# Kernel optimization log

Hardware: AMD Instinct MI355X
Metric: run time of the kernel (lower is better)

The kernel has to match this reference:

```python
import jax, jax.numpy as jnp
import numpy as np

B, S, D, H = 2, 2048, 1024, 16
DK = D // H


def setup_inputs() -> dict:
    key = jax.random.key(0)
    ks = jax.random.split(key, 12)
    scale = 0.02  # keep exp(QK^T) finite in fp32
    return {
        "query": jax.random.normal(ks[0], (B, S, D), jnp.float32),
        "key_": jax.random.normal(ks[1], (B, S, D), jnp.float32),
        "value": jax.random.normal(ks[2], (B, S, D), jnp.float32),
        "mask": jax.random.randint(ks[3], (B, S, S), 0, 2, jnp.int32),
        "Wq": scale * jax.random.normal(ks[4], (D, D), jnp.float32),
        "bq": jnp.zeros((D,), jnp.float32),
        "Wk": scale * jax.random.normal(ks[5], (D, D), jnp.float32),
        "bk": jnp.zeros((D,), jnp.float32),
        "Wv": scale * jax.random.normal(ks[6], (D, D), jnp.float32),
        "bv": jnp.zeros((D,), jnp.float32),
        "Wo": scale * jax.random.normal(ks[7], (D, D), jnp.float32),
        "bo": jnp.zeros((D,), jnp.float32),
    }


def reference(query, key_, value, mask, Wq, bq, Wk, bk, Wv, bv, Wo, bo):
    b, s, d = query.shape
    # torch Linear: x @ W.T + b, then split heads -> [b, h, s, d_k]
    def proj(x, W, bias):
        return (x @ W.T + bias).reshape(b, s, H, DK).transpose(0, 2, 1, 3)

    q = proj(query, Wq, bq)
    k = proj(key_, Wk, bk)
    v = proj(value, Wv, bv)

    # non-standard: exp(QK^T) / sqrt(d_k), then mask, then softmax
    scores = jnp.exp(jnp.einsum("bhqd,bhkd->bhqk", q, k)) / jnp.sqrt(
        jnp.asarray(DK, q.dtype)
    )
    scores = jnp.where(mask[:, None, :, :] == 0, jnp.asarray(-1e9, q.dtype), scores)
    p_attn = jax.nn.softmax(scores, axis=-1)

    out = jnp.einsum("bhqk,bhkd->bhqd", p_attn, v)  # [b, h, s, d_k]
    out = out.transpose(0, 2, 1, 3).reshape(b, s, d)  # merge heads
    return out @ Wo.T + bo
```

## Files before the change

### kernel.cpp

```cpp
#include <hip/hip_runtime.h>
#include <math.h>

#define B_ 2
#define S_ 2048
#define D_ 1024
#define H_ 16
#define DK_ 64
#define M_ (B_*S_)

typedef __attribute__((ext_vector_type(8))) _Float16 f16x8;
typedef __attribute__((ext_vector_type(4))) _Float16 f16x4;
typedef __attribute__((ext_vector_type(2))) __fp16 fp16x2;
typedef __attribute__((ext_vector_type(4))) float f32x4;

#define MFMA16(a,b,c) __builtin_amdgcn_mfma_f32_16x16x32_f16((a),(b),(c),0,0,0)

__device__ __forceinline__ void gload16(const void* g, void* l) {
    __builtin_amdgcn_global_load_lds(
        (const __attribute__((address_space(1))) unsigned int*)g,
        (__attribute__((address_space(3))) unsigned int*)l, 16, 0, 0);
}

__global__ __launch_bounds__(256)
void wsplit(const float* __restrict__ Wq, const float* __restrict__ Wk,
            const float* __restrict__ Wv, const float* __restrict__ Wo,
            _Float16* __restrict__ hq, _Float16* __restrict__ lq,
            _Float16* __restrict__ hk, _Float16* __restrict__ lk,
            _Float16* __restrict__ hv, _Float16* __restrict__ ho)
{
    int t = blockIdx.x * 256 + threadIdx.x;
    int mi = t >> 17;
    int e  = (t & 131071) * 8;
    const float* src = (mi == 0) ? Wq : (mi == 1) ? Wk : (mi == 2) ? Wv : Wo;
    float4 a = *(const float4*)&src[e];
    float4 b = *(const float4*)&src[e + 4];
    float v[8] = {a.x, a.y, a.z, a.w, b.x, b.y, b.z, b.w};
    f16x8 hi, lo;
    #pragma unroll
    for (int j = 0; j < 8; ++j) {
        float s = v[j] * 64.f;
        _Float16 h = (_Float16)s;
        hi[j] = h; lo[j] = (_Float16)(s - (float)h);
    }
    if (mi == 0)      { *(f16x8*)&hq[e] = hi; *(f16x8*)&lq[e] = lo; }
    else if (mi == 1) { *(f16x8*)&hk[e] = hi; *(f16x8*)&lk[e] = lo; }
    else if (mi == 2) { *(f16x8*)&hv[e] = hi; }
    else              { *(f16x8*)&ho[e] = hi; }
}

__global__ __launch_bounds__(256)
void maskpack(const int* __restrict__ mask, unsigned long long* __restrict__ mbits)
{
    int wid  = (blockIdx.x * 256 + threadIdx.x) >> 6;
    int lane = threadIdx.x & 63;
    int v = mask[(size_t)wid * 64 + lane];
    unsigned long long bal = __ballot(v != 0);
    if (lane == 0) mbits[wid] = bal;
}

template<int NPROD, int OUT_MODE>
__device__ __forceinline__
void gemm_body(char* smem, const float* __restrict__ Ap,
               const _Float16* __restrict__ Bhi, const _Float16* __restrict__ Blo,
               const float* __restrict__ bias, void* __restrict__ outp, int gid)
{
    _Float16* AhiS = (_Float16*)smem;
    _Float16* BhiS = (_Float16*)(smem + 8192);
    _Float16* AloS = (_Float16*)(smem + 16384);
    _Float16* BloS = (_Float16*)(smem + 24576);

    const int tid  = threadIdx.x;
    const int lane = tid & 63, w = tid >> 6;
    const int lx   = lane & 15, lg = lane >> 4;
    const int wm   = w >> 1, wn = w & 1;

    int nid = (gid & 7) * 32 + (gid >> 3);
    const int colBase = (nid & 7) * 128;
    const int rowBase = (nid >> 3) * 128;

    f32x4 acc[4][4];
    #pragma unroll
    for (int i = 0; i < 4; ++i)
        #pragma unroll
        for (int j = 0; j < 4; ++j) acc[i][j] = (f32x4){0.f, 0.f, 0.f, 0.f};

    const int sr = tid >> 1, sh = tid & 1;

    for (int k0 = 0; k0 < D_; k0 += 32) {
        __syncthreads();
        #pragma unroll
        for (int ii = 0; ii < 2; ++ii) {
            int i  = w * 2 + ii;
            int rr = i * 16 + (lane >> 2);
            int cc = (lane & 3) ^ ((lane >> 2) & 3);
            gload16(Bhi + (size_t)(colBase + rr) * D_ + k0 + cc * 8, &BhiS[i * 512]);
            if (NPROD == 3)
                gload16(Blo + (size_t)(colBase + rr) * D_ + k0 + cc * 8, &BloS[i * 512]);
        }
        {
            char* bp = (char*)AhiS + sr * 64;
            int c0 = sh * 2;
            const float* ap = Ap + (size_t)(rowBase + sr) * D_ + k0 + sh * 16;
            float4 x0 = *(const float4*)ap;
            float4 x1 = *(const float4*)(ap + 4);
            float4 x2 = *(const float4*)(ap + 8);
            float4 x3 = *(const float4*)(ap + 12);
            float xv[16] = {x0.x,x0.y,x0.z,x0.w, x1.x,x1.y,x1.z,x1.w,
                            x2.x,x2.y,x2.z,x2.w, x3.x,x3.y,x3.z,x3.w};
            f16x8 hi[2], lo[2];
            #pragma unroll
            for (int j = 0; j < 16; ++j) {
                _Float16 hv = (_Float16)xv[j];
                hi[j >> 3][j & 7] = hv;
                if (NPROD == 3) lo[j >> 3][j & 7] = (_Float16)(xv[j] - (float)hv);
            }
            *(f16x8*)(bp + 16 * ((c0 + 0) ^ (sr & 3))) = hi[0];
            *(f16x8*)(bp + 16 * ((c0 + 1) ^ (sr & 3))) = hi[1];
            if (NPROD == 3) {
                char* lp = (char*)AloS + sr * 64;
                *(f16x8*)(lp + 16 * ((c0 + 0) ^ (sr & 3))) = lo[0];
                *(f16x8*)(lp + 16 * ((c0 + 1) ^ (sr & 3))) = lo[1];
            }
        }
        __syncthreads();

        f16x8 bh[4], bl[4];
        #pragma unroll
        for (int fj = 0; fj < 4; ++fj) {
            int brow = wn * 64 + fj * 16 + lx;
            bh[fj] = *(const f16x8*)((char*)BhiS + brow * 64 + 16 * (lg ^ (brow & 3)));
            if (NPROD == 3)
                bl[fj] = *(const f16x8*)((char*)BloS + brow * 64 + 16 * (lg ^ (brow & 3)));
        }
        #pragma unroll
        for (int fi = 0; fi < 4; ++fi) {
            int arow = wm * 64 + fi * 16 + lx;
            f16x8 ah = *(const f16x8*)((char*)AhiS + arow * 64 + 16 * (lg ^ (arow & 3)));
            f16x8 al;
            if (NPROD == 3)
                al = *(const f16x8*)((char*)AloS + arow * 64 + 16 * (lg ^ (arow & 3)));
            #pragma unroll
            for (int fj = 0; fj < 4; ++fj) {
                acc[fi][fj] = MFMA16(ah, bh[fj], acc[fi][fj]);
                if (NPROD == 3) {
                    acc[fi][fj] = MFMA16(ah, bl[fj], acc[fi][fj]);
                    acc[fi][fj] = MFMA16(al, bh[fj], acc[fi][fj]);
                }
            }
        }
    }

    constexpr float INV = 1.f / 64.f;
    #pragma unroll
    for (int fi = 0; fi < 4; ++fi) {
        #pragma unroll
        for (int fj = 0; fj < 4; ++fj) {
            int n = colBase + wn * 64 + fj * 16 + lx;
            float bv = bias[n];
            if (OUT_MODE == 1) {
                _Float16* Ohi = (_Float16*)outp;
                _Float16* Olo = Ohi + (size_t)M_ * D_;
                int hh = n >> 6, d = n & 63;
                #pragma unroll
                for (int rr = 0; rr < 4; ++rr) {
                    int m = rowBase + wm * 64 + fi * 16 + lg * 4 + rr;
                    int bb = m >> 11, s = m & 2047;
                    float val = acc[fi][fj][rr] * INV + bv;
                    _Float16 hv = (_Float16)val;
                    size_t o = (((size_t)bb * H_ + hh) * S_ + s) * DK_ + d;
                    Ohi[o] = hv;
                    Olo[o] = (_Float16)(val - (float)hv);
                }
            } else {
                _Float16* Vt = (_Float16*)outp;
                int hh = n >> 6, d = n & 63;
                int m0 = rowBase + wm * 64 + fi * 16 + lg * 4;
                int bb = m0 >> 11, s = m0 & 2047;
                f16x4 pk;
                #pragma unroll
                for (int rr = 0; rr < 4; ++rr)
                    pk[rr] = (_Float16)(acc[fi][fj][rr] * INV + bv);
                *(f16x4*)&Vt[(((size_t)bb * H_ + hh) * DK_ + d) * S_ + s] = pk;
            }
        }
    }
}

__global__ __launch_bounds__(256)
void proj3(const float* __restrict__ query, const float* __restrict__ key_,
           const float* __restrict__ value,
           const _Float16* __restrict__ WhiQ, const _Float16* __restrict__ WloQ,
           const _Float16* __restrict__ WhiK, const _Float16* __restrict__ WloK,
           const _Float16* __restrict__ WhiV,
           const float* __restrict__ bq, const float* __restrict__ bk,
           const float* __restrict__ bv,
           _Float16* __restrict__ Qhi, _Float16* __restrict__ Khi,
           _Float16* __restrict__ VtW)
{
    extern __shared__ char smem[];
    int mode = blockIdx.x >> 8;
    int gid  = blockIdx.x & 255;
    if (mode == 0)
        gemm_body<3, 1>(smem, query, WhiQ, WloQ, bq, Qhi, gid);
    else if (mode == 1)
        gemm_body<3, 1>(smem, key_, WhiK, WloK, bk, Khi, gid);
    else
        gemm_body<1, 2>(smem, value, WhiV, nullptr, bv, VtW, gid);
}

__global__ __launch_bounds__(256)
void gemm64(const _Float16* __restrict__ Ap, const _Float16* __restrict__ Bhi,
            const float* __restrict__ bias, float* __restrict__ out)
{
    __shared__ __attribute__((aligned(16))) _Float16 AhiS[64 * 32];
    __shared__ __attribute__((aligned(16))) _Float16 BhiS[128 * 32];

    const int tid  = threadIdx.x;
    const int lane = tid & 63, w = tid >> 6;
    const int lx   = lane & 15, lg = lane >> 4;
    const int wm   = w >> 1, wn = w & 1;

    int gid = blockIdx.x;
    int nid = (gid & 7) * 64 + (gid >> 3);
    const int colBase = (nid & 7) * 128;
    const int rowBase = (nid >> 3) * 64;

    f32x4 acc[2][4];
    #pragma unroll
    for (int i = 0; i < 2; ++i)
        #pragma unroll
        for (int j = 0; j < 4; ++j) acc[i][j] = (f32x4){0.f, 0.f, 0.f, 0.f};

    const int sr = tid >> 2, sh = tid & 3;

    for (int k0 = 0; k0 < D_; k0 += 32) {
        __syncthreads();
        #pragma unroll
        for (int ii = 0; ii < 2; ++ii) {
            int i  = w * 2 + ii;
            int rr = i * 16 + (lane >> 2);
            int cc = (lane & 3) ^ ((lane >> 2) & 3);
            gload16(Bhi + (size_t)(colBase + rr) * D_ + k0 + cc * 8, &BhiS[i * 512]);
        }
        {
            const _Float16* ap = Ap + (size_t)(rowBase + sr) * D_ + k0 + sh * 8;
            f16x8 h0 = *(const f16x8*)ap;
            *(f16x8*)((char*)AhiS + sr * 64 + 16 * (sh ^ (sr & 3))) = h0;
        }
        __syncthreads();

        f16x8 bh[4];
        #pragma unroll
        for (int fj = 0; fj < 4; ++fj) {
            int brow = wn * 64 + fj * 16 + lx;
            bh[fj] = *(const f16x8*)((char*)BhiS + brow * 64 + 16 * (lg ^ (brow & 3)));
        }
        #pragma unroll
        for (int fi = 0; fi < 2; ++fi) {
            int arow = wm * 32 + fi * 16 + lx;
            f16x8 ah = *(const f16x8*)((char*)AhiS + arow * 64 + 16 * (lg ^ (arow & 3)));
            #pragma unroll
            for (int fj = 0; fj < 4; ++fj)
                acc[fi][fj] = MFMA16(ah, bh[fj], acc[fi][fj]);
        }
    }

    constexpr float INV = 1.f / 64.f;
    #pragma unroll
    for (int fi = 0; fi < 2; ++fi) {
        #pragma unroll
        for (int fj = 0; fj < 4; ++fj) {
            int n = colBase + wn * 64 + fj * 16 + lx;
            float bv = bias[n];
            #pragma unroll
            for (int rr = 0; rr < 4; ++rr) {
                int m = rowBase + wm * 32 + fi * 16 + lg * 4 + rr;
                out[(size_t)m * D_ + n] = acc[fi][fj][rr] * INV + bv;
            }
        }
    }
}

__global__ __launch_bounds__(512, 4)
void flash_mfma(const _Float16* __restrict__ Qhi, const _Float16* __restrict__ Qlo,
                const _Float16* __restrict__ Khi, const _Float16* __restrict__ Klo,
                const _Float16* __restrict__ Vt, const unsigned long long* __restrict__ Mb,
                _Float16* __restrict__ octx)
{
    __shared__ __attribute__((aligned(16))) _Float16 KhiS[64 * 64];
    __shared__ __attribute__((aligned(16))) _Float16 KloS[64 * 64];
    __shared__ __attribute__((aligned(16))) _Float16 VtS[64 * 64];
    __shared__ __attribute__((aligned(16))) _Float16 PwS[8][16 * 64];

    const int tid  = threadIdx.x;
    const int lane = tid & 63;
    const int w    = tid >> 6;
    const int lx   = lane & 15;
    const int lg   = lane >> 4;

    int bid = blockIdx.x;
    int swz = (bid & 7) * 64 + (bid >> 3);
    int qb = swz & 15;
    int h  = (swz >> 4) & 15;
    int b  = swz >> 8;

    const int q0 = qb * 128;
    const size_t bh = (size_t)b * H_ + h;
    const _Float16* KhiG = Khi + bh * S_ * DK_;
    const _Float16* KloG = Klo + bh * S_ * DK_;
    const _Float16* VtG  = Vt  + bh * DK_ * S_;

    const int qrow = q0 + w * 16 + lx;
    f16x8 qh[2], ql[2];
    {
        const _Float16* ph = Qhi + bh * S_ * DK_ + (size_t)qrow * DK_ + lg * 8;
        const _Float16* pl = Qlo + bh * S_ * DK_ + (size_t)qrow * DK_ + lg * 8;
        qh[0] = *(const f16x8*)ph;
        qh[1] = *(const f16x8*)(ph + 32);
        ql[0] = *(const f16x8*)pl;
        ql[1] = *(const f16x8*)(pl + 32);
    }

    f32x4 oacc[4];
    float m_run = -1e30f, l_run = 0.f;
    #pragma unroll
    for (int dt = 0; dt < 4; ++dt) oacc[dt] = (f32x4){0.f, 0.f, 0.f, 0.f};

    char* Pw = (char*)&PwS[w][0];
    const unsigned long long* mrow = Mb + ((size_t)b * S_ + qrow) * (S_ / 64);

    for (int s0 = 0; s0 < S_; s0 += 64) {
        __syncthreads();

        {
            int rr = w * 8 + (lane >> 3);
            int cc = (lane & 7) ^ (lane >> 3);
            gload16(KhiG + (size_t)(s0 + rr) * DK_ + cc * 8, &KhiS[w * 512]);
            gload16(KloG + (size_t)(s0 + rr) * DK_ + cc * 8, &KloS[w * 512]);
            gload16(VtG + (size_t)rr * S_ + s0 + cc * 8, &VtS[w * 512]);
        }
        unsigned long long mw = mrow[s0 >> 6];
        __syncthreads();

        float sv[4][4];
        #pragma unroll
        for (int ct = 0; ct < 4; ++ct) {
            int row  = ct * 16 + lx;
            int sw   = (row & 7) << 4;
            int base = row * 128 + lg * 16;
            f16x8 kh0 = *(const f16x8*)((const char*)KhiS + ((base +  0) ^ sw));
            f16x8 kh1 = *(const f16x8*)((const char*)KhiS + ((base + 64) ^ sw));
            f16x8 kl0 = *(const f16x8*)((const char*)KloS + ((base +  0) ^ sw));
            f16x8 kl1 = *(const f16x8*)((const char*)KloS + ((base + 64) ^ sw));
            f32x4 s = (f32x4){0.f, 0.f, 0.f, 0.f};
            s = MFMA16(kh0, qh[0], s);
            s = MFMA16(kh1, qh[1], s);
            s = MFMA16(kl0, qh[0], s);
            s = MFMA16(kl1, qh[1], s);
            s = MFMA16(kh0, ql[0], s);
            s = MFMA16(kh1, ql[1], s);
            #pragma unroll
            for (int r = 0; r < 4; ++r) sv[ct][r] = s[r];
        }

        unsigned long long ms = mw >> (lg * 4);
        float tv[16];
        #pragma unroll
        for (int ct = 0; ct < 4; ++ct)
            #pragma unroll
            for (int r = 0; r < 4; ++r) {
                float e = __expf(sv[ct][r] - 2.0794415416798357f);
                tv[ct * 4 + r] = ((ms >> (ct * 16 + r)) & 1ull) ? e : -1e30f;
            }
        float m01 = fmaxf(fmaxf(tv[0], tv[1]), fmaxf(tv[2], tv[3]));
        float m23 = fmaxf(fmaxf(tv[4], tv[5]), fmaxf(tv[6], tv[7]));
        float m45 = fmaxf(fmaxf(tv[8], tv[9]), fmaxf(tv[10], tv[11]));
        float m67 = fmaxf(fmaxf(tv[12], tv[13]), fmaxf(tv[14], tv[15]));
        float tmax = fmaxf(fmaxf(m01, m23), fmaxf(m45, m67));
        tmax = fmaxf(tmax, __shfl_xor(tmax, 16));
        tmax = fmaxf(tmax, __shfl_xor(tmax, 32));

        if (__any(tmax > m_run)) {
            float mn = fmaxf(m_run, tmax);
            float scl = __expf(m_run - mn);
            m_run = mn;
            l_run *= scl;
            #pragma unroll
            for (int dt = 0; dt < 4; ++dt)
                #pragma unroll
                for (int r = 0; r < 4; ++r) oacc[dt][r] *= scl;
        }
        float mr = m_run;
        float pp[16], sum = 0.f;
        #pragma unroll
        for (int i = 0; i < 16; ++i) {
            pp[i] = __expf(tv[i] - mr);
            sum += pp[i];
        }
        sum += __shfl_xor(sum, 16);
        sum += __shfl_xor(sum, 32);
        l_run += sum;

        {
            int psw = (lx & 7) << 4;
            #pragma unroll
            for (int ct = 0; ct < 4; ++ct) {
                fp16x2 a = __builtin_amdgcn_cvt_pkrtz(pp[ct * 4 + 0], pp[ct * 4 + 1]);
                fp16x2 c = __builtin_amdgcn_cvt_pkrtz(pp[ct * 4 + 2], pp[ct * 4 + 3]);
                unsigned int au, cu;
                __builtin_memcpy(&au, &a, 4);
                __builtin_memcpy(&cu, &c, 4);
                int off = lx * 128 + ct * 32 + lg * 8;
                *(unsigned int*)(Pw + ((off + 0) ^ psw)) = au;
                *(unsigned int*)(Pw + ((off + 4) ^ psw)) = cu;
            }
        }

        f16x8 pa0, pa1;
        {
            int psw = (lx & 7) << 4;
            int pb  = lx * 128 + lg * 16;
            pa0 = *(const f16x8*)(Pw + ((pb +  0) ^ psw));
            pa1 = *(const f16x8*)(Pw + ((pb + 64) ^ psw));
        }
        #pragma unroll
        for (int dt = 0; dt < 4; ++dt) {
            int vrow = dt * 16 + lx;
            int vs   = (vrow & 7) << 4;
            int vb   = vrow * 128 + lg * 16;
            f16x8 v0 = *(const f16x8*)((const char*)VtS + ((vb +  0) ^ vs));
            f16x8 v1 = *(const f16x8*)((const char*)VtS + ((vb + 64) ^ vs));
            oacc[dt] = MFMA16(v0, pa0, oacc[dt]);
            oacc[dt] = MFMA16(v1, pa1, oacc[dt]);
        }
    }

    {
        float inv = 1.0f / l_run;
        #pragma unroll
        for (int dt = 0; dt < 4; ++dt) {
            f16x4 o;
            #pragma unroll
            for (int r = 0; r < 4; ++r) o[r] = (_Float16)(oacc[dt][r] * inv);
            *(f16x4*)&octx[((size_t)b * S_ + qrow) * D_ + h * DK_ + dt * 16 + lg * 4] = o;
        }
    }
}

extern "C" void kernel_launch(void* const* d_in, const int* in_sizes, int n_in,
                              void* d_out, int out_size, void* d_ws, size_t ws_size,
                              hipStream_t stream)
{
    const float* query = (const float*)d_in[0];
    const float* key_  = (const float*)d_in[1];
    const float* value = (const float*)d_in[2];
    const int*   mask  = (const int*)d_in[3];
    const float* Wq = (const float*)d_in[4];
    const float* bq = (const float*)d_in[5];
    const float* Wk = (const float*)d_in[6];
    const float* bk = (const float*)d_in[7];
    const float* Wv = (const float*)d_in[8];
    const float* bv = (const float*)d_in[9];
    const float* Wo = (const float*)d_in[10];
    const float* bo = (const float*)d_in[11];

    char* p = (char*)d_ws;
    unsigned long long* mbits = (unsigned long long*)p;  p += (size_t)1 << 20;
    _Float16* WhiQ = (_Float16*)p;  p += (size_t)2 << 20;
    _Float16* WloQ = (_Float16*)p;  p += (size_t)2 << 20;
    _Float16* WhiK = (_Float16*)p;  p += (size_t)2 << 20;
    _Float16* WloK = (_Float16*)p;  p += (size_t)2 << 20;
    _Float16* WhiV = (_Float16*)p;  p += (size_t)2 << 20;
    _Float16* WhiO = (_Float16*)p;  p += (size_t)2 << 20;
    _Float16* Qhi  = (_Float16*)p;  p += (size_t)8 << 20;
    _Float16* Qlo  = (_Float16*)p;  p += (size_t)8 << 20;
    _Float16* Khi  = (_Float16*)p;  p += (size_t)8 << 20;
    _Float16* Klo  = (_Float16*)p;  p += (size_t)8 << 20;
    _Float16* VtW  = (_Float16*)p;  p += (size_t)8 << 20;
    _Float16* octx = (_Float16*)p;  p += (size_t)8 << 20;
    float* out = (float*)d_out;
    (void)Qlo; (void)Klo;

    maskpack<<<(B_ * S_ * (S_ / 64) * 64) / 256, 256, 0, stream>>>(mask, mbits);
    wsplit<<<2048, 256, 0, stream>>>(Wq, Wk, Wv, Wo,
                                     WhiQ, WloQ, WhiK, WloK, WhiV, WhiO);

    proj3<<<768, 256, 32768, stream>>>(query, key_, value,
                                       WhiQ, WloQ, WhiK, WloK, WhiV,
                                       bq, bk, bv, Qhi, Khi, VtW);

    flash_mfma<<<512, 512, 0, stream>>>(Qhi, Qlo, Khi, Klo, VtW, mbits, octx);

    gemm64<<<512, 256, 0, stream>>>(octx, WhiO, bo, out);
}
```

Before: 225.1 us.

## Pre-split activations to fp16 and double-buffer LDS staging in projection GEMMs

Activations (query/key/value) are now pre-converted to fp16 hi/lo pairs, with a 64x scale, in a merged split kernel. The projection GEMM can then stage both A and B through async global_load_lds instead of converting fp32 in registers on every k-step. Both the projection GEMM and the output GEMM switch to double-buffered LDS, prefetching the next k-tile while computing the current one, which also removes one barrier per iteration. The cost is an extra full pass over the activations to write the fp16 copies, plus twice the LDS per block, which may lower occupancy. Qlo/Klo are now placed right after Qhi/Khi to match the OUT_MODE layout.

```diff
diff --git a/kernel.cpp b/kernel.cpp
--- a/kernel.cpp
+++ b/kernel.cpp
@@ -22,16 +22,33 @@
 }
 
 __global__ __launch_bounds__(256)
-void wsplit(const float* __restrict__ Wq, const float* __restrict__ Wk,
-            const float* __restrict__ Wv, const float* __restrict__ Wo,
-            _Float16* __restrict__ hq, _Float16* __restrict__ lq,
-            _Float16* __restrict__ hk, _Float16* __restrict__ lk,
-            _Float16* __restrict__ hv, _Float16* __restrict__ ho)
+void splitall(const float* __restrict__ query, const float* __restrict__ key_,
+              const float* __restrict__ value,
+              const float* __restrict__ Wq, const float* __restrict__ Wk,
+              const float* __restrict__ Wv, const float* __restrict__ Wo,
+              _Float16* __restrict__ Xhq, _Float16* __restrict__ Xlq,
+              _Float16* __restrict__ Xhk, _Float16* __restrict__ Xlk,
+              _Float16* __restrict__ Xhv,
+              _Float16* __restrict__ hq, _Float16* __restrict__ lq,
+              _Float16* __restrict__ hk, _Float16* __restrict__ lk,
+              _Float16* __restrict__ hv, _Float16* __restrict__ ho)
 {
     int t = blockIdx.x * 256 + threadIdx.x;
-    int mi = t >> 17;
-    int e  = (t & 131071) * 8;
-    const float* src = (mi == 0) ? Wq : (mi == 1) ? Wk : (mi == 2) ? Wv : Wo;
+    int region = t >> 19;
+    int u = t & 524287;
+    const float* src; _Float16* dhi; _Float16* dlo; size_t e;
+    if (region < 3) {
+        e = (size_t)u * 8;
+        src = (region == 0) ? query : (region == 1) ? key_ : value;
+        dhi = (region == 0) ? Xhq : (region == 1) ? Xhk : Xhv;
+        dlo = (region == 0) ? Xlq : (region == 1) ? Xlk : nullptr;
+    } else {
+        int mi = u >> 17;
+        e = (size_t)(u & 131071) * 8;
+        src = (mi == 0) ? Wq : (mi == 1) ? Wk : (mi == 2) ? Wv : Wo;
+        dhi = (mi == 0) ? hq : (mi == 1) ? hk : (mi == 2) ? hv : ho;
+        dlo = (mi == 0) ? lq : (mi == 1) ? lk : nullptr;
+    }
     float4 a = *(const float4*)&src[e];
     float4 b = *(const float4*)&src[e + 4];
     float v[8] = {a.x, a.y, a.z, a.w, b.x, b.y, b.z, b.w};
@@ -42,10 +59,8 @@
         _Float16 h = (_Float16)s;
         hi[j] = h; lo[j] = (_Float16)(s - (float)h);
     }
-    if (mi == 0)      { *(f16x8*)&hq[e] = hi; *(f16x8*)&lq[e] = lo; }
-    else if (mi == 1) { *(f16x8*)&hk[e] = hi; *(f16x8*)&lk[e] = lo; }
-    else if (mi == 2) { *(f16x8*)&hv[e] = hi; }
-    else              { *(f16x8*)&ho[e] = hi; }
+    *(f16x8*)&dhi[e] = hi;
+    if (dlo) *(f16x8*)&dlo[e] = lo;
 }
 
 __global__ __launch_bounds__(256)
@@ -60,15 +75,12 @@
 
 template<int NPROD, int OUT_MODE>
 __device__ __forceinline__
-void gemm_body(char* smem, const float* __restrict__ Ap,
-               const _Float16* __restrict__ Bhi, const _Float16* __restrict__ Blo,
-               const float* __restrict__ bias, void* __restrict__ outp, int gid)
-{
-    _Float16* AhiS = (_Float16*)smem;
-    _Float16* BhiS = (_Float16*)(smem + 8192);
-    _Float16* AloS = (_Float16*)(smem + 16384);
-    _Float16* BloS = (_Float16*)(smem + 24576);
-
+void gemm_body2(char* smem, const _Float16* __restrict__ Ah,
+                const _Float16* __restrict__ Al,
+                const _Float16* __restrict__ Bh, const _Float16* __restrict__ Bl,
+                const float* __restrict__ bias, void* __restrict__ outp, int gid)
+{
+    constexpr int BUFSZ = (NPROD == 3) ? 32768 : 16384;
     const int tid  = threadIdx.x;
     const int lane = tid & 63, w = tid >> 6;
     const int lx   = lane & 15, lg = lane >> 4;
@@ -78,67 +90,56 @@
     const int colBase = (nid & 7) * 128;
     const int rowBase = (nid >> 3) * 128;
 
+    const int sRow = (lane >> 2);
+    const int sChk = (lane & 3) ^ ((lane >> 2) & 3);
+
+    auto STAGE = [&](int buf, int k0) {
+        char* base = smem + buf * BUFSZ;
+        #pragma unroll
+        for (int ii = 0; ii < 2; ++ii) {
+            int i = w * 2 + ii;
+            int r = i * 16 + sRow;
+            gload16(Ah + (size_t)(rowBase + r) * D_ + k0 + sChk * 8, base + i * 1024);
+            gload16(Bh + (size_t)(colBase + r) * D_ + k0 + sChk * 8, base + 8192 + i * 1024);
+            if (NPROD == 3) {
+                gload16(Al + (size_t)(rowBase + r) * D_ + k0 + sChk * 8, base + 16384 + i * 1024);
+                gload16(Bl + (size_t)(colBase + r) * D_ + k0 + sChk * 8, base + 24576 + i * 1024);
+            }
+        }
+    };
+
     f32x4 acc[4][4];
     #pragma unroll
     for (int i = 0; i < 4; ++i)
         #pragma unroll
         for (int j = 0; j < 4; ++j) acc[i][j] = (f32x4){0.f, 0.f, 0.f, 0.f};
 
-    const int sr = tid >> 1, sh = tid & 1;
-
+    STAGE(0, 0);
+    __syncthreads();
+    int cur = 0;
     for (int k0 = 0; k0 < D_; k0 += 32) {
-        __syncthreads();
-        #pragma unroll
-        for (int ii = 0; ii < 2; ++ii) {
-            int i  = w * 2 + ii;
-            int rr = i * 16 + (lane >> 2);
-            int cc = (lane & 3) ^ ((lane >> 2) & 3);
-            gload16(Bhi + (size_t)(colBase + rr) * D_ + k0 + cc * 8, &BhiS[i * 512]);
-            if (NPROD == 3)
-                gload16(Blo + (size_t)(colBase + rr) * D_ + k0 + cc * 8, &BloS[i * 512]);
-        }
-        {
-            char* bp = (char*)AhiS + sr * 64;
-            int c0 = sh * 2;
-            const float* ap = Ap + (size_t)(rowBase + sr) * D_ + k0 + sh * 16;
-            float4 x0 = *(const float4*)ap;
-            float4 x1 = *(const float4*)(ap + 4);
-            float4 x2 = *(const float4*)(ap + 8);
-            float4 x3 = *(const float4*)(ap + 12);
-            float xv[16] = {x0.x,x0.y,x0.z,x0.w, x1.x,x1.y,x1.z,x1.w,
-                            x2.x,x2.y,x2.z,x2.w, x3.x,x3.y,x3.z,x3.w};
-            f16x8 hi[2], lo[2];
-            #pragma unroll
-            for (int j = 0; j < 16; ++j) {
-                _Float16 hv = (_Float16)xv[j];
-                hi[j >> 3][j & 7] = hv;
-                if (NPROD == 3) lo[j >> 3][j & 7] = (_Float16)(xv[j] - (float)hv);
-            }
-            *(f16x8*)(bp + 16 * ((c0 + 0) ^ (sr & 3))) = hi[0];
-            *(f16x8*)(bp + 16 * ((c0 + 1) ^ (sr & 3))) = hi[1];
-            if (NPROD == 3) {
-                char* lp = (char*)AloS + sr * 64;
-                *(f16x8*)(lp + 16 * ((c0 + 0) ^ (sr & 3))) = lo[0];
-                *(f16x8*)(lp + 16 * ((c0 + 1) ^ (sr & 3))) = lo[1];
-            }
-        }
-        __syncthreads();
+        if (k0 + 32 < D_) STAGE(cur ^ 1, k0 + 32);
+        char* base = smem + cur * BUFSZ;
+        _Float16* AhS = (_Float16*)base;
+        _Float16* BhS = (_Float16*)(base + 8192);
+        _Float16* AlS = (_Float16*)(base + 16384);
+        _Float16* BlS = (_Float16*)(base + 24576);
 
         f16x8 bh[4], bl[4];
         #pragma unroll
         for (int fj = 0; fj < 4; ++fj) {
             int brow = wn * 64 + fj * 16 + lx;
-            bh[fj] = *(const f16x8*)((char*)BhiS + brow * 64 + 16 * (lg ^ (brow & 3)));
+            bh[fj] = *(const f16x8*)((char*)BhS + brow * 64 + 16 * (lg ^ (brow & 3)));
             if (NPROD == 3)
-                bl[fj] = *(const f16x8*)((char*)BloS + brow * 64 + 16 * (lg ^ (brow & 3)));
+                bl[fj] = *(const f16x8*)((char*)BlS + brow * 64 + 16 * (lg ^ (brow & 3)));
         }
         #pragma unroll
         for (int fi = 0; fi < 4; ++fi) {
             int arow = wm * 64 + fi * 16 + lx;
-            f16x8 ah = *(const f16x8*)((char*)AhiS + arow * 64 + 16 * (lg ^ (arow & 3)));
+            f16x8 ah = *(const f16x8*)((char*)AhS + arow * 64 + 16 * (lg ^ (arow & 3)));
             f16x8 al;
             if (NPROD == 3)
-                al = *(const f16x8*)((char*)AloS + arow * 64 + 16 * (lg ^ (arow & 3)));
+                al = *(const f16x8*)((char*)AlS + arow * 64 + 16 * (lg ^ (arow & 3)));
             #pragma unroll
             for (int fj = 0; fj < 4; ++fj) {
                 acc[fi][fj] = MFMA16(ah, bh[fj], acc[fi][fj]);
@@ -148,9 +149,11 @@
                 }
             }
         }
-    }
-
-    constexpr float INV = 1.f / 64.f;
+        __syncthreads();
+        cur ^= 1;
+    }
+
+    constexpr float INV = 1.f / 4096.f;
     #pragma unroll
     for (int fi = 0; fi < 4; ++fi) {
         #pragma unroll
@@ -187,8 +190,9 @@
 }
 
 __global__ __launch_bounds__(256)
-void proj3(const float* __restrict__ query, const float* __restrict__ key_,
-           const float* __restrict__ value,
+void proj3(const _Float16* __restrict__ Xhq, const _Float16* __restrict__ Xlq,
+           const _Float16* __restrict__ Xhk, const _Float16* __restrict__ Xlk,
+           const _Float16* __restrict__ Xhv,
            const _Float16* __restrict__ WhiQ, const _Float16* __restrict__ WloQ,
            const _Float16* __restrict__ WhiK, const _Float16* __restrict__ WloK,
            const _Float16* __restrict__ WhiV,
@@ -201,19 +205,18 @@
     int mode = blockIdx.x >> 8;
     int gid  = blockIdx.x & 255;
     if (mode == 0)
-        gemm_body<3, 1>(smem, query, WhiQ, WloQ, bq, Qhi, gid);
+        gemm_body2<3, 1>(smem, Xhq, Xlq, WhiQ, WloQ, bq, Qhi, gid);
     else if (mode == 1)
-        gemm_body<3, 1>(smem, key_, WhiK, WloK, bk, Khi, gid);
+        gemm_body2<3, 1>(smem, Xhk, Xlk, WhiK, WloK, bk, Khi, gid);
     else
-        gemm_body<1, 2>(smem, value, WhiV, nullptr, bv, VtW, gid);
+        gemm_body2<1, 2>(smem, Xhv, nullptr, WhiV, nullptr, bv, VtW, gid);
 }
 
 __global__ __launch_bounds__(256)
 void gemm64(const _Float16* __restrict__ Ap, const _Float16* __restrict__ Bhi,
             const float* __restrict__ bias, float* __restrict__ out)
 {
-    __shared__ __attribute__((aligned(16))) _Float16 AhiS[64 * 32];
-    __shared__ __attribute__((aligned(16))) _Float16 BhiS[128 * 32];
+    __shared__ __attribute__((aligned(16))) char smem[24576];
 
     const int tid  = threadIdx.x;
     const int lane = tid & 63, w = tid >> 6;
@@ -225,44 +228,53 @@
     const int colBase = (nid & 7) * 128;
     const int rowBase = (nid >> 3) * 64;
 
+    const int sRow = (lane >> 2);
+    const int sChk = (lane & 3) ^ ((lane >> 2) & 3);
+
+    auto STAGE = [&](int buf, int k0) {
+        char* base = smem + buf * 12288;
+        gload16(Ap + (size_t)(rowBase + w * 16 + sRow) * D_ + k0 + sChk * 8,
+                base + w * 1024);
+        #pragma unroll
+        for (int ii = 0; ii < 2; ++ii) {
+            int i = w * 2 + ii;
+            int r = i * 16 + sRow;
+            gload16(Bhi + (size_t)(colBase + r) * D_ + k0 + sChk * 8,
+                    base + 4096 + i * 1024);
+        }
+    };
+
     f32x4 acc[2][4];
     #pragma unroll
     for (int i = 0; i < 2; ++i)
         #pragma unroll
         for (int j = 0; j < 4; ++j) acc[i][j] = (f32x4){0.f, 0.f, 0.f, 0.f};
 
-    const int sr = tid >> 2, sh = tid & 3;
-
+    STAGE(0, 0);
+    __syncthreads();
+    int cur = 0;
     for (int k0 = 0; k0 < D_; k0 += 32) {
-        __syncthreads();
-        #pragma unroll
-        for (int ii = 0; ii < 2; ++ii) {
-            int i  = w * 2 + ii;
-            int rr = i * 16 + (lane >> 2);
-            int cc = (lane & 3) ^ ((lane >> 2) & 3);
-            gload16(Bhi + (size_t)(colBase + rr) * D_ + k0 + cc * 8, &BhiS[i * 512]);
-        }
-        {
-            const _Float16* ap = Ap + (size_t)(rowBase + sr) * D_ + k0 + sh * 8;
-            f16x8 h0 = *(const f16x8*)ap;
-            *(f16x8*)((char*)AhiS + sr * 64 + 16 * (sh ^ (sr & 3))) = h0;
-        }
-        __syncthreads();
+        if (k0 + 32 < D_) STAGE(cur ^ 1, k0 + 32);
+        char* base = smem + cur * 12288;
+        _Float16* AS = (_Float16*)base;
+        _Float16* BS = (_Float16*)(base + 4096);
 
         f16x8 bh[4];
         #pragma unroll
         for (int fj = 0; fj < 4; ++fj) {
             int brow = wn * 64 + fj * 16 + lx;
-            bh[fj] = *(const f16x8*)((char*)BhiS + brow * 64 + 16 * (lg ^ (brow & 3)));
+            bh[fj] = *(const f16x8*)((char*)BS + brow * 64 + 16 * (lg ^ (brow & 3)));
         }
         #pragma unroll
         for (int fi = 0; fi < 2; ++fi) {
             int arow = wm * 32 + fi * 16 + lx;
-            f16x8 ah = *(const f16x8*)((char*)AhiS + arow * 64 + 16 * (lg ^ (arow & 3)));
+            f16x8 ah = *(const f16x8*)((char*)AS + arow * 64 + 16 * (lg ^ (arow & 3)));
             #pragma unroll
             for (int fj = 0; fj < 4; ++fj)
                 acc[fi][fj] = MFMA16(ah, bh[fj], acc[fi][fj]);
         }
+        __syncthreads();
+        cur ^= 1;
     }
 
     constexpr float INV = 1.f / 64.f;
@@ -472,20 +484,26 @@
     _Float16* WloK = (_Float16*)p;  p += (size_t)2 << 20;
     _Float16* WhiV = (_Float16*)p;  p += (size_t)2 << 20;
     _Float16* WhiO = (_Float16*)p;  p += (size_t)2 << 20;
-    _Float16* Qhi  = (_Float16*)p;  p += (size_t)8 << 20;
-    _Float16* Qlo  = (_Float16*)p;  p += (size_t)8 << 20;
-    _Float16* Khi  = (_Float16*)p;  p += (size_t)8 << 20;
-    _Float16* Klo  = (_Float16*)p;  p += (size_t)8 << 20;
+    _Float16* Xhq  = (_Float16*)p;  p += (size_t)8 << 20;
+    _Float16* Xlq  = (_Float16*)p;  p += (size_t)8 << 20;
+    _Float16* Xhk  = (_Float16*)p;  p += (size_t)8 << 20;
+    _Float16* Xlk  = (_Float16*)p;  p += (size_t)8 << 20;
+    _Float16* Xhv  = (_Float16*)p;  p += (size_t)8 << 20;
+    _Float16* Qhi  = (_Float16*)p;  p += (size_t)16 << 20;
+    _Float16* Khi  = (_Float16*)p;  p += (size_t)16 << 20;
     _Float16* VtW  = (_Float16*)p;  p += (size_t)8 << 20;
     _Float16* octx = (_Float16*)p;  p += (size_t)8 << 20;
     float* out = (float*)d_out;
-    (void)Qlo; (void)Klo;
+
+    _Float16* Qlo = Qhi + (size_t)M_ * D_;
+    _Float16* Klo = Khi + (size_t)M_ * D_;
 
     maskpack<<<(B_ * S_ * (S_ / 64) * 64) / 256, 256, 0, stream>>>(mask, mbits);
-    wsplit<<<2048, 256, 0, stream>>>(Wq, Wk, Wv, Wo,
-                                     WhiQ, WloQ, WhiK, WloK, WhiV, WhiO);
-
-    proj3<<<768, 256, 32768, stream>>>(query, key_, value,
+    splitall<<<8192, 256, 0, stream>>>(query, key_, value, Wq, Wk, Wv, Wo,
+                                       Xhq, Xlq, Xhk, Xlk, Xhv,
+                                       WhiQ, WloQ, WhiK, WloK, WhiV, WhiO);
+
+    proj3<<<768, 256, 65536, stream>>>(Xhq, Xlq, Xhk, Xlk, Xhv,
                                        WhiQ, WloQ, WhiK, WloK, WhiV,
                                        bq, bk, bv, Qhi, Khi, VtW);
 
```

After: 211.0 us. -6.3%, faster.
